# Kernel optimization log

Hardware: AMD Instinct MI355X
Metric: run time of the kernel (lower is better)

Reference implementation:

```python
import jax, jax.numpy as jnp
import numpy as np

C = 128  # num_hidden[-1]; nheads = 1 so dim == C
L, H, W = 16, 96, 96


def conv5(x, w):
    # x: [N, Cin, H, W], w: [1, Cin, 5, 5]; padding=2 -> SAME
    return jax.lax.conv_general_dilated(
        x, w, window_strides=(1, 1), padding=[(2, 2), (2, 2)],
        dimension_numbers=('NCHW', 'OIHW', 'NCHW'))


def setup_inputs() -> dict:
    key = jax.random.key(0)
    ks = jax.random.split(key, 9)
    s = 0.05
    return dict(
        x=jax.random.normal(ks[0], (L, C, H, W), jnp.float32),
        Wq=jax.random.normal(ks[1], (C, C), jnp.float32) * s,
        bq=jax.random.normal(ks[2], (C,), jnp.float32) * s,
        Wk=jax.random.normal(ks[3], (C, C), jnp.float32) * s,
        bk=jax.random.normal(ks[4], (C,), jnp.float32) * s,
        Wv=jax.random.normal(ks[5], (C, C), jnp.float32) * s,
        bv=jax.random.normal(ks[6], (C,), jnp.float32) * s,
        Wa=jax.random.normal(ks[7], (1, 2 * C, 5, 5), jnp.float32) * s,
        ba=jax.random.normal(ks[8], (1,), jnp.float32) * s,
    )


def reference(x, Wq, bq, Wk, bk, Wv, bv, Wa, ba):
    # 1x1 convs == per-pixel linear maps
    Q = jnp.einsum('lchw,dc->ldhw', x, Wq) + bq[None, :, None, None]
    K = jnp.einsum('lchw,dc->ldhw', x, Wk) + bk[None, :, None, None]
    V = jnp.einsum('lchw,dc->ldhw', x, Wv) + bv[None, :, None, None]
    # conv5x5(cat(Qi, Kj)) = conv5x5(Qi; Wa_q) + conv5x5(Kj; Wa_k) + ba
    Aq = conv5(Q, Wa[:, :C])[:, 0]   # [L, H, W]
    Ak = conv5(K, Wa[:, C:])[:, 0]   # [L, H, W]
    S = Aq[:, None] + Ak[None, :] + ba[0]       # [L, L, H, W] score maps H_ij
    A = jax.nn.softmax(S, axis=1)               # softmax over key frame j
    out = jnp.einsum('ijhw,jchw->ichw', A, V)   # weighted sum of V over j
    return out
```

## Files before the change

kernel.cpp:

```cpp
#include <hip/hip_runtime.h>


#define HW    9216
#define HDIM  96
#define WDIM  96
#define CDIM  128
#define WP    28

__device__ __forceinline__ void fma4(float4& a, const float4& x, const float4& s) {
    a.x += x.x * s.x; a.y += x.y * s.y; a.z += x.z * s.z; a.w += x.w * s.w;
}
__device__ __forceinline__ void axpy4(float4& o, float w, const float4& v) {
    o.x += w * v.x; o.y += w * v.y; o.z += w * v.z; o.w += w * v.w;
}

__global__ void k_prep(const float* __restrict__ Wk, const float* __restrict__ Wa,
                       const float* __restrict__ Wv,
                       float* __restrict__ weffp, float* __restrict__ wvt) {
    const int b = blockIdx.x;
    if (b < 14) {
        int idx = b * 256 + threadIdx.x;
        if (idx < 128 * WP) {
            int cp = idx / WP, tap = idx % WP;
            float s = 0.f;
            if (tap < 25)
                for (int c = 0; c < 128; ++c)
                    s += Wk[c * 128 + cp] * Wa[(128 + c) * 25 + tap];
            weffp[idx] = s;
        }
    } else {
        int idx = (b - 14) * 256 + threadIdx.x;
        wvt[(idx & 127) * 128 + (idx >> 7)] = Wv[idx];
    }
}

__global__ __launch_bounds__(256) void k_z(const float* __restrict__ x,
                                           const float* __restrict__ weffp,
                                           float* __restrict__ z) {
    __shared__ float red[4][25][128];
    const int tid  = threadIdx.x;
    const int wav  = __builtin_amdgcn_readfirstlane(tid >> 6);
    const int lane = tid & 63;
    const int j    = blockIdx.y;
    const int px0  = blockIdx.x * 128;

    const float* wg = weffp + wav * 32 * WP;
    const float* xb = x + ((size_t)j * CDIM + wav * 32) * HW + px0 + 2 * lane;

    float2 acc[25];
    #pragma unroll
    for (int t = 0; t < 25; ++t) acc[t] = make_float2(0.f, 0.f);

    #pragma unroll 8
    for (int c = 0; c < 32; ++c) {
        float2 xv = *(const float2*)(xb + (size_t)c * HW);
        #pragma unroll
        for (int t = 0; t < 25; ++t) {
            float wv = wg[c * WP + t];
            acc[t].x = fmaf(wv, xv.x, acc[t].x);
            acc[t].y = fmaf(wv, xv.y, acc[t].y);
        }
    }

    #pragma unroll
    for (int t = 0; t < 25; ++t)
        *(float2*)(&red[wav][t][2 * lane]) = acc[t];
    __syncthreads();

    float* zb = z + (size_t)j * 25 * HW + px0;
    #pragma unroll
    for (int it = 0; it < 4; ++it) {
        int idx = it * 256 + tid;
        if (idx < 800) {
            int t = idx >> 5, q = (idx & 31) * 4;
            float4 s0 = *(const float4*)(&red[0][t][q]);
            float4 s1 = *(const float4*)(&red[1][t][q]);
            float4 s2 = *(const float4*)(&red[2][t][q]);
            float4 s3 = *(const float4*)(&red[3][t][q]);
            float4 s;
            s.x = (s0.x + s1.x) + (s2.x + s3.x);
            s.y = (s0.y + s1.y) + (s2.y + s3.y);
            s.z = (s0.z + s1.z) + (s2.z + s3.z);
            s.w = (s0.w + s1.w) + (s2.w + s3.w);
            *(float4*)(zb + (size_t)t * HW + q) = s;
        }
    }
}

__global__ __launch_bounds__(256) void k_ak(const float* __restrict__ z,
                                            float* __restrict__ ak) {
    const int j  = blockIdx.y;
    const int px = (blockIdx.x * 256 + threadIdx.x) * 4;
    const int h  = px / WDIM, cb = px % WDIM;
    const bool cok0 = (cb > 0);
    const bool cok2 = (cb < WDIM - 4);
    const float4 zf = make_float4(0.f, 0.f, 0.f, 0.f);
    const float* zb = z + (size_t)j * 25 * HW + px;

    float s0 = 0.f, s1 = 0.f, s2 = 0.f, s3 = 0.f;
    #pragma unroll
    for (int kh = 0; kh < 5; ++kh) {
        const bool rok = (unsigned)(h + kh - 2) < (unsigned)HDIM;
        const float* rp = zb + (kh * 5) * HW + (kh - 2) * WDIM;
        #pragma unroll
        for (int kw = 0; kw < 5; ++kw) {
            const float* tp = rp + kw * HW;
            float4 qa = (rok && cok0) ? *(const float4*)(tp - 4) : zf;
            float4 qb = (rok        ) ? *(const float4*)(tp)     : zf;
            float4 qc = (rok && cok2) ? *(const float4*)(tp + 4) : zf;
            float win[12] = {qa.x, qa.y, qa.z, qa.w, qb.x, qb.y, qb.z, qb.w,
                             qc.x, qc.y, qc.z, qc.w};
            s0 += win[kw + 2];
            s1 += win[kw + 3];
            s2 += win[kw + 4];
            s3 += win[kw + 5];
        }
    }
    float4 o = make_float4(s0, s1, s2, s3);
    *(float4*)(ak + (size_t)j * HW + px) = o;
}

__global__ __launch_bounds__(192) void k_conv(const float* __restrict__ x,
                                              const float* __restrict__ weffp,
                                              float* __restrict__ part) {
    const int j  = blockIdx.x;
    const int rt = blockIdx.y;
    const int g  = blockIdx.z;
    const int c0 = g * 16;
    __shared__ float tile[36 * 104];
    __shared__ float wsm[16 * WP];
    const int tid = threadIdx.x;
    for (int i = tid; i < 16 * WP; i += 192) wsm[i] = weffp[c0 * WP + i];
    const int cq = tid % 24;
    const int rg = tid / 24;
    const int r0 = rg * 4;
    const int rowbase = rt * 32;

    float4 acc[4];
    acc[0] = acc[1] = acc[2] = acc[3] = make_float4(0.f, 0.f, 0.f, 0.f);

    for (int ch = 0; ch < 16; ++ch) {
        const float* xc = x + (size_t)(j * CDIM + c0 + ch) * HW;
        __syncthreads();
        for (int idx = tid; idx < 36 * 26; idx += 192) {
            int r = idx / 26, q = idx % 26;
            int gr = rowbase - 2 + r;
            int gc = q * 4 - 4;
            float4 v = make_float4(0.f, 0.f, 0.f, 0.f);
            if (gr >= 0 && gr < HDIM && gc >= 0 && gc < WDIM)
                v = *(const float4*)(xc + gr * WDIM + gc);
            *(float4*)(tile + r * 104 + q * 4) = v;
        }
        __syncthreads();
        const float* wc = wsm + ch * WP;
        for (int rr = 0; rr < 8; ++rr) {
            const float* trow = tile + (r0 + rr) * 104 + cq * 4;
            float4 a  = *(const float4*)(trow);
            float4 b  = *(const float4*)(trow + 4);
            float4 c4 = *(const float4*)(trow + 8);
            float win[12] = {a.x, a.y, a.z, a.w, b.x, b.y, b.z, b.w,
                             c4.x, c4.y, c4.z, c4.w};
            #pragma unroll
            for (int orow = 0; orow < 4; ++orow) {
                int kh = rr - orow;
                if (kh < 0 || kh > 4) continue;
                #pragma unroll
                for (int kw = 0; kw < 5; ++kw) {
                    float w = wc[kh * 5 + kw];
                    acc[orow].x += w * win[kw + 2];
                    acc[orow].y += w * win[kw + 3];
                    acc[orow].z += w * win[kw + 4];
                    acc[orow].w += w * win[kw + 5];
                }
            }
        }
    }
    float* pr = part + (size_t)(g * 16 + j) * HW;
    #pragma unroll
    for (int orow = 0; orow < 4; ++orow) {
        int row = rowbase + r0 + orow;
        *(float4*)(pr + row * WDIM + cq * 4) = acc[orow];
    }
}

__global__ void k_combine(const float* __restrict__ part, float* __restrict__ ak) {
    const int j  = blockIdx.y;
    const int px = blockIdx.x * 256 + threadIdx.x;
    float s = 0.f;
    #pragma unroll
    for (int g = 0; g < 8; ++g) s += part[(size_t)(g * 16 + j) * HW + px];
    ak[(size_t)j * HW + px] = s;
}

__global__ __launch_bounds__(256) void k_xbar(const float* __restrict__ x,
                                              const float* __restrict__ ak,
                                              float* __restrict__ xbar) {
    const int b  = blockIdx.x;
    const int cp = b / 9;
    const int px = (b % 9) * 1024 + threadIdx.x * 4;

    float4 av[16];
    #pragma unroll
    for (int j = 0; j < 16; ++j)
        av[j] = *(const float4*)(ak + (size_t)j * HW + px);

    float4 m = av[0];
    #pragma unroll
    for (int j = 1; j < 16; ++j) {
        m.x = fmaxf(m.x, av[j].x); m.y = fmaxf(m.y, av[j].y);
        m.z = fmaxf(m.z, av[j].z); m.w = fmaxf(m.w, av[j].w);
    }
    float4 tot = make_float4(0.f, 0.f, 0.f, 0.f);
    #pragma unroll
    for (int j = 0; j < 16; ++j) {
        av[j].x = __expf(av[j].x - m.x); av[j].y = __expf(av[j].y - m.y);
        av[j].z = __expf(av[j].z - m.z); av[j].w = __expf(av[j].w - m.w);
        tot.x += av[j].x; tot.y += av[j].y; tot.z += av[j].z; tot.w += av[j].w;
    }
    float4 inv = make_float4(1.f / tot.x, 1.f / tot.y, 1.f / tot.z, 1.f / tot.w);

    float4 acc = make_float4(0.f, 0.f, 0.f, 0.f);
    #pragma unroll
    for (int j = 0; j < 16; ++j) {
        float4 xv = *(const float4*)(x + (size_t)(j * CDIM + cp) * HW + px);
        fma4(acc, xv, av[j]);
    }
    acc.x *= inv.x; acc.y *= inv.y; acc.z *= inv.z; acc.w *= inv.w;
    *(float4*)(xbar + (size_t)cp * HW + px) = acc;
}

__global__ __launch_bounds__(256) void k_mat(const float* __restrict__ xbar,
                                             const float* __restrict__ wvt,
                                             const float* __restrict__ bv,
                                             float* __restrict__ out) {
    __shared__ float lx[128 * 16];
    const int b    = blockIdx.x;
    const int half = blockIdx.y;
    const int tile = (b & 7) * 72 + (b >> 3);
    const int px0  = tile * 16;
    const int tid  = threadIdx.x;

    #pragma unroll
    for (int i = 0; i < 2; ++i) {
        int lin = tid + i * 256;
        int cp = lin >> 2, q = lin & 3;
        *(float4*)(lx + cp * 16 + q * 4) =
            *(const float4*)(xbar + (size_t)cp * HW + px0 + q * 4);
    }
    __syncthreads();

    const int q = tid & 3;
    const int c = half * 64 + (tid >> 2);
    float4 o = make_float4(0.f, 0.f, 0.f, 0.f);
    #pragma unroll 4
    for (int cp = 0; cp < 128; ++cp) {
        float4 xv = *(const float4*)(lx + cp * 16 + q * 4);
        axpy4(o, wvt[cp * 128 + c], xv);
    }
    float bb = bv[c];
    o.x += bb; o.y += bb; o.z += bb; o.w += bb;

    for (int i = 0; i < 16; ++i) {
        float* ob = out + (size_t)(i * CDIM + c) * HW + px0 + q * 4;
        *(float4*)(ob) = o;
    }
}

extern "C" void kernel_launch(void* const* d_in, const int* in_sizes, int n_in,
                              void* d_out, int out_size, void* d_ws, size_t ws_size,
                              hipStream_t stream) {
    const float* x  = (const float*)d_in[0];
    const float* Wk = (const float*)d_in[3];
    const float* Wv = (const float*)d_in[5];
    const float* bv = (const float*)d_in[6];
    const float* Wa = (const float*)d_in[7];
    float* out = (float*)d_out;

    char* ws = (char*)d_ws;
    float* weffp = (float*)(ws);
    float* wvt   = (float*)(ws + 16384);

    k_prep<<<78, 256, 0, stream>>>(Wk, Wa, Wv, weffp, wvt);

    const size_t Z_BYTES  = (size_t)16 * 25 * HW * 4;
    const size_t AK_BYTES = (size_t)16 * HW * 4;
    const size_t NEED_BIG = 81920 + Z_BYTES + AK_BYTES;

    if (ws_size >= NEED_BIG) {
        float* z   = (float*)(ws + 81920);
        float* akb = (float*)(ws + 81920 + Z_BYTES);
        float* xb  = (float*)(ws + 81920);
        k_z   <<<dim3(72, 16),  256, 0, stream>>>(x, weffp, z);
        k_ak  <<<dim3(9, 16),   256, 0, stream>>>(z, akb);
        k_xbar<<<1152,          256, 0, stream>>>(x, akb, xb);
        k_mat <<<dim3(576, 2),  256, 0, stream>>>(xb, wvt, bv, out);
    } else {
        float* part = (float*)(ws + 81920);
        float* akb  = (float*)(ws + 81920 + 4718592);
        float* xb   = (float*)(ws + 81920);
        k_conv   <<<dim3(16, 3, 8), 192, 0, stream>>>(x, weffp, part);
        k_combine<<<dim3(36, 16),   256, 0, stream>>>(part, akb);
        k_xbar   <<<1152,           256, 0, stream>>>(x, akb, xb);
        k_mat    <<<dim3(576, 2),   256, 0, stream>>>(xb, wvt, bv, out);
    }
}
```

Measured before the change: 80.31 us.

## Compute full channel reduction per thread in k_z, dropping split-channel LDS reduction

k_z now has each thread handle one pixel across all 128 channels, accumulating 25 tap sums in registers and writing them directly. This replaces the previous scheme where four waves each reduced 32 channels for two pixels and then combined results through shared memory with a barrier. It removes the LDS traffic and sync but halves the grid to 576 blocks, with a longer serial loop per thread and scalar instead of float2 loads.

```diff
diff --git a/kernel.cpp b/kernel.cpp
--- a/kernel.cpp
+++ b/kernel.cpp
@@ -37,54 +37,25 @@
 __global__ __launch_bounds__(256) void k_z(const float* __restrict__ x,
                                            const float* __restrict__ weffp,
                                            float* __restrict__ z) {
-    __shared__ float red[4][25][128];
-    const int tid  = threadIdx.x;
-    const int wav  = __builtin_amdgcn_readfirstlane(tid >> 6);
-    const int lane = tid & 63;
-    const int j    = blockIdx.y;
-    const int px0  = blockIdx.x * 128;
-
-    const float* wg = weffp + wav * 32 * WP;
-    const float* xb = x + ((size_t)j * CDIM + wav * 32) * HW + px0 + 2 * lane;
-
-    float2 acc[25];
-    #pragma unroll
-    for (int t = 0; t < 25; ++t) acc[t] = make_float2(0.f, 0.f);
-
-    #pragma unroll 8
-    for (int c = 0; c < 32; ++c) {
-        float2 xv = *(const float2*)(xb + (size_t)c * HW);
+    const int j  = blockIdx.y;
+    const int px = blockIdx.x * 256 + threadIdx.x;
+    const float* xb = x + (size_t)j * CDIM * HW + px;
+
+    float acc[25];
+    #pragma unroll
+    for (int t = 0; t < 25; ++t) acc[t] = 0.f;
+
+    #pragma unroll 16
+    for (int c = 0; c < 128; ++c) {
+        float xv = xb[(size_t)c * HW];
         #pragma unroll
-        for (int t = 0; t < 25; ++t) {
-            float wv = wg[c * WP + t];
-            acc[t].x = fmaf(wv, xv.x, acc[t].x);
-            acc[t].y = fmaf(wv, xv.y, acc[t].y);
-        }
-    }
-
-    #pragma unroll
-    for (int t = 0; t < 25; ++t)
-        *(float2*)(&red[wav][t][2 * lane]) = acc[t];
-    __syncthreads();
-
-    float* zb = z + (size_t)j * 25 * HW + px0;
-    #pragma unroll
-    for (int it = 0; it < 4; ++it) {
-        int idx = it * 256 + tid;
-        if (idx < 800) {
-            int t = idx >> 5, q = (idx & 31) * 4;
-            float4 s0 = *(const float4*)(&red[0][t][q]);
-            float4 s1 = *(const float4*)(&red[1][t][q]);
-            float4 s2 = *(const float4*)(&red[2][t][q]);
-            float4 s3 = *(const float4*)(&red[3][t][q]);
-            float4 s;
-            s.x = (s0.x + s1.x) + (s2.x + s3.x);
-            s.y = (s0.y + s1.y) + (s2.y + s3.y);
-            s.z = (s0.z + s1.z) + (s2.z + s3.z);
-            s.w = (s0.w + s1.w) + (s2.w + s3.w);
-            *(float4*)(zb + (size_t)t * HW + q) = s;
-        }
-    }
+        for (int t = 0; t < 25; ++t)
+            acc[t] = fmaf(weffp[c * WP + t], xv, acc[t]);
+    }
+
+    float* zb = z + (size_t)j * 25 * HW + px;
+    #pragma unroll
+    for (int t = 0; t < 25; ++t) zb[(size_t)t * HW] = acc[t];
 }
 
 __global__ __launch_bounds__(256) void k_ak(const float* __restrict__ z,
@@ -290,7 +261,7 @@
         float* z   = (float*)(ws + 81920);
         float* akb = (float*)(ws + 81920 + Z_BYTES);
         float* xb  = (float*)(ws + 81920);
-        k_z   <<<dim3(72, 16),  256, 0, stream>>>(x, weffp, z);
+        k_z   <<<dim3(36, 16),  256, 0, stream>>>(x, weffp, z);
         k_ak  <<<dim3(9, 16),   256, 0, stream>>>(z, akb);
         k_xbar<<<1152,          256, 0, stream>>>(x, akb, xb);
         k_mat <<<dim3(576, 2),  256, 0, stream>>>(xb, wvt, bv, out);
```

Result: slower. 89.94 us (+12.0%).
